# Kernel optimization log

Measured on AMD Instinct MI355X. Metric: run time of the kernel, lower is better.

The kernel has to match this reference:

```python
import jax, jax.numpy as jnp
import numpy as np

SEQ_LEN = 4096
DIM_HALF = 2048  # x last dim = 2 * DIM_HALF
DIM_OUT = 1024
LN_EPS = 1e-5


def setup_inputs() -> dict:
    key = jax.random.key(0)
    k1, k2, k3 = jax.random.split(key, 3)
    x = jax.random.normal(k1, (SEQ_LEN, 2 * DIM_HALF), dtype=jnp.float32)
    ln_scale = jnp.ones((DIM_HALF,), dtype=jnp.float32)
    # original init is uniform(-eps/n, eps/n); scale randn similarly small
    spatial_weights = jax.random.normal(k2, (SEQ_LEN, SEQ_LEN), dtype=jnp.float32) * (0.001 / SEQ_LEN)
    spatial_biases = jnp.ones((SEQ_LEN, 1), dtype=jnp.float32)
    proj_w = jax.random.normal(k3, (DIM_HALF, DIM_OUT), dtype=jnp.float32) * (1.0 / np.sqrt(DIM_HALF))
    proj_b = jnp.zeros((DIM_OUT,), dtype=jnp.float32)
    return {"x": x, "ln_scale": ln_scale, "spatial_weights": spatial_weights,
            "spatial_biases": spatial_biases, "proj_w": proj_w, "proj_b": proj_b}


def reference(x, ln_scale, spatial_weights, spatial_biases, proj_w, proj_b):
    # split into value half and gate half
    xh, gate = jnp.split(x, 2, axis=-1)  # each (n, d)
    # LayerNorm (scale only, no offset), haiku default eps=1e-5
    mean = jnp.mean(gate, axis=-1, keepdims=True)
    var = jnp.var(gate, axis=-1, keepdims=True)
    gate = (gate - mean) * jax.lax.rsqrt(var + LN_EPS) * ln_scale
    # causal (lower-triangular) masked spatial mixing: out[m,d] = sum_n w[m,n] * gate[n,d]
    n = spatial_weights.shape[0]
    w = jnp.tril(spatial_weights)
    gate = jnp.einsum('nd,mn->md', gate, w) + spatial_biases  # (n, d)
    # gating multiply + output projection
    out = (xh * gate) @ proj_w + proj_b  # (n, dim_out)
    return out
```

## Files before the change

### kernel.cpp

```cpp
#include <hip/hip_runtime.h>
#include <cstdint>
#include <cstddef>

#define SEQ 4096
#define DH 2048
#define DOUT 1024

typedef float f32x4 __attribute__((ext_vector_type(4)));
typedef __bf16 bf16x8 __attribute__((ext_vector_type(8)));
typedef long longx2 __attribute__((ext_vector_type(2)));


__device__ __forceinline__ unsigned short f2bf(float f) {
  unsigned int u = __float_as_uint(f);
  unsigned int r = (u + 0x7FFFu + ((u >> 16) & 1u)) >> 16;
  return (unsigned short)r;
}

__device__ __forceinline__ unsigned char f2f8(float f) {
  unsigned int u = __float_as_uint(f);
  unsigned int sign = (u >> 24) & 0x80u;
  float a = __uint_as_float(u & 0x7FFFFFFFu);
  if (a >= 448.f) return (unsigned char)(sign | 0x7Eu);
  if (a < 0.015625f) {
    int q = (int)rintf(a * 512.0f);
    if (q == 8) return (unsigned char)(sign | 0x08u);
    return (unsigned char)(sign | (unsigned)q);
  }
  int e = (int)((u >> 23) & 0xFF) - 127;
  unsigned int m = u & 0x7FFFFFu;
  unsigned int m3 = (m + 0x7FFFFu + ((m >> 20) & 1u)) >> 20;
  if (m3 == 8u) { m3 = 0u; e++; if (e > 8) return (unsigned char)(sign | 0x7Eu); }
  return (unsigned char)(sign | ((unsigned)(e + 7) << 3) | m3);
}

__device__ __forceinline__ void g2l16(const void* g, void* l) {
  __builtin_amdgcn_global_load_lds((__attribute__((address_space(1))) void*)g,
                                   (__attribute__((address_space(3))) void*)l, 16, 0, 0);
}

#define W_SCALE 1048576.0f
#define W_SCALE_INV (1.0f / 1048576.0f)


__global__ __launch_bounds__(256) void prep_all(const float* __restrict__ x,
                                                float* __restrict__ mv,
                                                float* __restrict__ rv,
                                                const float* __restrict__ w,
                                                unsigned char* __restrict__ wf8,
                                                const float* __restrict__ pw,
                                                unsigned short* __restrict__ pT) {
  int b = blockIdx.x;
  if (b < 4096) {
    int row = b;
    const float4* g4 = (const float4*)(x + (size_t)row * (2 * DH) + DH);
    float4 a = g4[threadIdx.x];
    float4 bb = g4[threadIdx.x + 256];
    float s  = a.x + a.y + a.z + a.w + bb.x + bb.y + bb.z + bb.w;
    float s2 = a.x * a.x + a.y * a.y + a.z * a.z + a.w * a.w +
               bb.x * bb.x + bb.y * bb.y + bb.z * bb.z + bb.w * bb.w;
#pragma unroll
    for (int o = 32; o > 0; o >>= 1) {
      s  += __shfl_down(s, o);
      s2 += __shfl_down(s2, o);
    }
    __shared__ float red[8];
    int wave = threadIdx.x >> 6;
    if ((threadIdx.x & 63) == 0) { red[wave] = s; red[wave + 4] = s2; }
    __syncthreads();
    if (threadIdx.x == 0) {
      float S  = red[0] + red[1] + red[2] + red[3];
      float S2 = red[4] + red[5] + red[6] + red[7];
      float mean = S * (1.0f / DH);
      float var  = S2 * (1.0f / DH) - mean * mean;
      mv[row] = mean;
      rv[row] = rsqrtf(var + 1e-5f);
    }
  } else if (b < 8192) {
    size_t e = (((size_t)(b - 4096)) * 256 + threadIdx.x) * 16;
    int m = (int)(e >> 12);
    int k = (int)(e & 4095);
    uint4 o;
    if (k > m) {
      o.x = o.y = o.z = o.w = 0u;
    } else {
      const float4* s4 = (const float4*)(w + e);
      float4 v0 = s4[0], v1 = s4[1], v2 = s4[2], v3 = s4[3];
      float vv[16] = {v0.x, v0.y, v0.z, v0.w, v1.x, v1.y, v1.z, v1.w,
                      v2.x, v2.y, v2.z, v2.w, v3.x, v3.y, v3.z, v3.w};
      unsigned char t[16];
#pragma unroll
      for (int j = 0; j < 16; j++)
        t[j] = (k + j <= m) ? f2f8(vv[j] * W_SCALE) : (unsigned char)0;
      o.x = (unsigned)t[0] | ((unsigned)t[1] << 8) | ((unsigned)t[2] << 16) | ((unsigned)t[3] << 24);
      o.y = (unsigned)t[4] | ((unsigned)t[5] << 8) | ((unsigned)t[6] << 16) | ((unsigned)t[7] << 24);
      o.z = (unsigned)t[8] | ((unsigned)t[9] << 8) | ((unsigned)t[10] << 16) | ((unsigned)t[11] << 24);
      o.w = (unsigned)t[12] | ((unsigned)t[13] << 8) | ((unsigned)t[14] << 16) | ((unsigned)t[15] << 24);
    }
    *(uint4*)(wf8 + e) = o;
  } else {
    __shared__ float tile[64][65];
    int b2 = b - 8192;
    int j0 = (b2 & 15) * 64;
    int d0 = (b2 >> 4) * 64;
#pragma unroll
    for (int i = 0; i < 16; i++) {
      int idx = threadIdx.x + i * 256;
      int r = idx >> 6, c = idx & 63;
      tile[r][c] = pw[(size_t)(d0 + r) * DOUT + j0 + c];
    }
    __syncthreads();
#pragma unroll
    for (int i = 0; i < 16; i++) {
      int idx = threadIdx.x + i * 256;
      int jr = idx >> 6, dc = idx & 63;
      pT[(size_t)(j0 + jr) * DH + d0 + dc] = f2bf(tile[dc][jr]);
    }
  }
}


__global__ __launch_bounds__(256) void norm_tr8(const float* __restrict__ x,
                                                const float* __restrict__ mv,
                                                const float* __restrict__ rv,
                                                const float* __restrict__ lns,
                                                unsigned char* __restrict__ gf8T) {
  __shared__ float tile[64][65];
  int d0 = blockIdx.x * 64;
  int n0 = blockIdx.y * 64;
#pragma unroll
  for (int i = 0; i < 16; i++) {
    int idx = threadIdx.x + i * 256;
    int r = idx >> 6, c = idx & 63;
    float v = x[(size_t)(n0 + r) * (2 * DH) + DH + d0 + c];
    tile[r][c] = (v - mv[n0 + r]) * rv[n0 + r];
  }
  __syncthreads();
#pragma unroll
  for (int i = 0; i < 4; i++) {
    int idx = threadIdx.x + i * 256;
    int dr = idx >> 4;
    int nq = idx & 15;
    float sc = lns[d0 + dr];
    unsigned int pk = 0;
#pragma unroll
    for (int j = 0; j < 4; j++)
      pk |= (unsigned int)f2f8(tile[nq * 4 + j][dr] * sc) << (8 * j);
    *(unsigned int*)&gf8T[(size_t)(d0 + dr) * SEQ + n0 + nq * 4] = pk;
  }
}


__global__ __launch_bounds__(256) void gemm_f8(const unsigned char* __restrict__ A,
                                               const unsigned char* __restrict__ BT,
                                               const float* __restrict__ xfull,
                                               const float* __restrict__ rbias,
                                               unsigned short* __restrict__ Pout) {
  constexpr int BK = 128;
  constexpr int ASZ = 64 * BK;
  __shared__ unsigned char sA[2 * ASZ];
  __shared__ unsigned char sB[2 * ASZ];

  const int tid = threadIdx.x;
  const int lane = tid & 63, wave = tid >> 6;
  const int quad = lane >> 4, l16 = lane & 15;
  const int wm = wave >> 1, wn = wave & 1;
  const int K = SEQ;

  const int lin = blockIdx.x;
  const int sw = ((lin & 7) << 7) | (lin >> 3);
  const int bn0 = (sw >> 5) * 64;
  const int by0 = sw & 31;

  for (int pass = 0; pass < 2; pass++) {
    const int by = pass == 0 ? by0 : 63 - by0;
    const int bm0 = by * 64;
    const int nt = (by + 2) >> 1;

    const unsigned char* aP[2];
    const unsigned char* bP[2];
#pragma unroll
    for (int r = 0; r < 2; r++) {
      int idx = r * 256 + tid;
      int row = idx >> 3;
      int col = ((idx & 7) ^ (row & 7)) * 16;
      aP[r] = A + (size_t)(bm0 + row) * K + col;
      bP[r] = BT + (size_t)(bn0 + row) * K + col;
    }

    f32x4 acc[2][2] = {};

    auto stage = [&](int buf) {
#pragma unroll
      for (int r = 0; r < 2; r++) {
        g2l16(aP[r], &sA[buf * ASZ + (r * 256 + tid) * 16]);
        aP[r] += BK;
      }
#pragma unroll
      for (int r = 0; r < 2; r++) {
        g2l16(bP[r], &sB[buf * ASZ + (r * 256 + tid) * 16]);
        bP[r] += BK;
      }
    };

    auto compute = [&](int buf) {
      const unsigned char* bA = &sA[buf * ASZ];
      const unsigned char* bB = &sB[buf * ASZ];
      long a8[4][2], b8[4][2];
#pragma unroll
      for (int i = 0; i < 2; i++) {
        int R = wm * 32 + i * 16 + l16;
        const unsigned char* rowp = &bA[R * BK];
        int s = R & 7;
        longx2 X = *(const longx2*)&rowp[(quad ^ s) * 16];
        longx2 Y = *(const longx2*)&rowp[((quad + 4) ^ s) * 16];
        a8[0][i] = X[0]; a8[1][i] = X[1]; a8[2][i] = Y[0]; a8[3][i] = Y[1];
      }
#pragma unroll
      for (int j = 0; j < 2; j++) {
        int R = wn * 32 + j * 16 + l16;
        const unsigned char* rowp = &bB[R * BK];
        int s = R & 7;
        longx2 X = *(const longx2*)&rowp[(quad ^ s) * 16];
        longx2 Y = *(const longx2*)&rowp[((quad + 4) ^ s) * 16];
        b8[0][j] = X[0]; b8[1][j] = X[1]; b8[2][j] = Y[0]; b8[3][j] = Y[1];
      }
#pragma unroll
      for (int h = 0; h < 4; h++)
#pragma unroll
        for (int i = 0; i < 2; i++)
#pragma unroll
          for (int j = 0; j < 2; j++)
            acc[i][j] = __builtin_amdgcn_mfma_f32_16x16x32_fp8_fp8(a8[h][i], b8[h][j], acc[i][j], 0, 0, 0);
    };

    stage(0);
    int cur = 0;
    for (int t = 0; t < nt; t++) {
      if (t + 1 < nt) {
        stage(cur ^ 1);
        asm volatile("s_waitcnt vmcnt(4)" ::: "memory");
      } else {
        asm volatile("s_waitcnt vmcnt(0)" ::: "memory");
      }
      __builtin_amdgcn_s_barrier();
      compute(cur);
      __builtin_amdgcn_s_barrier();
      cur ^= 1;
    }

#pragma unroll
    for (int i = 0; i < 2; i++) {
#pragma unroll
      for (int j = 0; j < 2; j++) {
        int col = bn0 + wn * 32 + j * 16 + l16;
#pragma unroll
        for (int r = 0; r < 4; r++) {
          int row = bm0 + wm * 32 + i * 16 + quad * 4 + r;
          float g = acc[i][j][r] * W_SCALE_INV + rbias[row];
          float pv = xfull[(size_t)row * (2 * DH) + col] * g;
          Pout[(size_t)row * DH + col] = f2bf(pv);
        }
      }
    }
  }
}


__global__ __launch_bounds__(256) void gemm_bf(const unsigned short* __restrict__ A,
                                               const unsigned short* __restrict__ BT,
                                               const float* __restrict__ cbias,
                                               float* __restrict__ out,
                                               int N, int K) {
  constexpr int BK = 64;
  constexpr int ASZ = 64 * BK;
  __shared__ unsigned short sA[2 * ASZ];
  __shared__ unsigned short sB[2 * ASZ];

  const int tid = threadIdx.x;
  const int lane = tid & 63, wave = tid >> 6;
  const int quad = lane >> 4, l16 = lane & 15;
  const int wm = wave >> 1, wn = wave & 1;

  const int lin = blockIdx.x;
  const int sw = ((lin & 7) << 7) | (lin >> 3);
  const int bn0 = (sw & 15) * 64;
  const int bm0 = (sw >> 4) * 64;
  const int nt = K / BK;

  const unsigned short* aP[2];
  const unsigned short* bP[2];
#pragma unroll
  for (int r = 0; r < 2; r++) {
    int idx = r * 256 + tid;
    int row = idx >> 3;
    int col = ((idx & 7) ^ (row & 7)) * 8;
    aP[r] = A + (size_t)(bm0 + row) * K + col;
    bP[r] = BT + (size_t)(bn0 + row) * K + col;
  }

  f32x4 acc[2][2] = {};

  auto stage = [&](int buf) {
#pragma unroll
    for (int r = 0; r < 2; r++) {
      g2l16(aP[r], &sA[buf * ASZ + (r * 256 + tid) * 8]);
      aP[r] += BK;
    }
#pragma unroll
    for (int r = 0; r < 2; r++) {
      g2l16(bP[r], &sB[buf * ASZ + (r * 256 + tid) * 8]);
      bP[r] += BK;
    }
  };

  auto compute = [&](int buf) {
    const unsigned short* bA = &sA[buf * ASZ];
    const unsigned short* bB = &sB[buf * ASZ];
    bf16x8 af[2][2], bfr[2][2];
#pragma unroll
    for (int h = 0; h < 2; h++) {
#pragma unroll
      for (int i = 0; i < 2; i++) {
        int R = wm * 32 + i * 16 + l16;
        af[h][i] = *(const bf16x8*)&bA[R * BK + (((h * 4 + quad) ^ (R & 7)) * 8)];
      }
#pragma unroll
      for (int j = 0; j < 2; j++) {
        int R = wn * 32 + j * 16 + l16;
        bfr[h][j] = *(const bf16x8*)&bB[R * BK + (((h * 4 + quad) ^ (R & 7)) * 8)];
      }
    }
#pragma unroll
    for (int h = 0; h < 2; h++)
#pragma unroll
      for (int i = 0; i < 2; i++)
#pragma unroll
        for (int j = 0; j < 2; j++)
          acc[i][j] = __builtin_amdgcn_mfma_f32_16x16x32_bf16(af[h][i], bfr[h][j], acc[i][j], 0, 0, 0);
  };

  stage(0);
  int cur = 0;
  for (int t = 0; t < nt; t++) {
    if (t + 1 < nt) {
      stage(cur ^ 1);
      asm volatile("s_waitcnt vmcnt(4)" ::: "memory");
    } else {
      asm volatile("s_waitcnt vmcnt(0)" ::: "memory");
    }
    __builtin_amdgcn_s_barrier();
    compute(cur);
    __builtin_amdgcn_s_barrier();
    cur ^= 1;
  }

#pragma unroll
  for (int i = 0; i < 2; i++) {
#pragma unroll
    for (int j = 0; j < 2; j++) {
      int col = bn0 + wn * 32 + j * 16 + l16;
#pragma unroll
      for (int r = 0; r < 4; r++) {
        int row = bm0 + wm * 32 + i * 16 + quad * 4 + r;
        out[(size_t)row * N + col] = acc[i][j][r] + cbias[col];
      }
    }
  }
}


extern "C" void kernel_launch(void* const* d_in, const int* in_sizes, int n_in,
                              void* d_out, int out_size, void* d_ws, size_t ws_size,
                              hipStream_t stream) {
  (void)in_sizes; (void)n_in; (void)out_size; (void)ws_size;
  const float* x   = (const float*)d_in[0];
  const float* lns = (const float*)d_in[1];
  const float* w   = (const float*)d_in[2];
  const float* sb  = (const float*)d_in[3];
  const float* pw  = (const float*)d_in[4];
  const float* pb  = (const float*)d_in[5];
  float* out = (float*)d_out;

  char* p = (char*)d_ws;
  unsigned char*  wf8   = (unsigned char*)p;  p += (size_t)SEQ * SEQ;
  unsigned char*  gf8T  = (unsigned char*)p;  p += (size_t)DH * SEQ;
  unsigned short* projT = (unsigned short*)p; p += (size_t)DOUT * DH * 2;
  unsigned short* Pbuf  = (unsigned short*)p; p += (size_t)SEQ * DH * 2;
  float* mv = (float*)p; p += (size_t)SEQ * 4;
  float* rv = (float*)p; p += (size_t)SEQ * 4;

  prep_all<<<4096 + 4096 + 512, 256, 0, stream>>>(x, mv, rv, w, wf8, pw, projT);
  norm_tr8<<<dim3(DH / 64, SEQ / 64), 256, 0, stream>>>(x, mv, rv, lns, gf8T);

  gemm_f8<<<1024, 256, 0, stream>>>(wf8, gf8T, x, sb, Pbuf);

  gemm_bf<<<1024, 256, 0, stream>>>(Pbuf, projT, pb, out, DOUT, DH);
}
```

Before: 232.6 us.

## Use hardware fp8 pack conversion and merge normalize-transpose into weight prep kernel

```diff
diff --git a/kernel.cpp b/kernel.cpp
--- a/kernel.cpp
+++ b/kernel.cpp
@@ -17,7 +17,7 @@
   return (unsigned short)r;
 }
 
-__device__ __forceinline__ unsigned char f2f8(float f) {
+__device__ __forceinline__ unsigned char f2f8_sw(float f) {
   unsigned int u = __float_as_uint(f);
   unsigned int sign = (u >> 24) & 0x80u;
   float a = __uint_as_float(u & 0x7FFFFFFFu);
@@ -34,6 +34,17 @@
   return (unsigned char)(sign | ((unsigned)(e + 7) << 3) | m3);
 }
 
+__device__ __forceinline__ unsigned int pk4_f8(float a, float b, float c, float d) {
+#if __has_builtin(__builtin_amdgcn_cvt_pk_fp8_f32)
+  int r = __builtin_amdgcn_cvt_pk_fp8_f32(a, b, 0, false);
+  r = __builtin_amdgcn_cvt_pk_fp8_f32(c, d, r, true);
+  return (unsigned int)r;
+#else
+  return (unsigned)f2f8_sw(a) | ((unsigned)f2f8_sw(b) << 8) |
+         ((unsigned)f2f8_sw(c) << 16) | ((unsigned)f2f8_sw(d) << 24);
+#endif
+}
+
 __device__ __forceinline__ void g2l16(const void* g, void* l) {
   __builtin_amdgcn_global_load_lds((__attribute__((address_space(1))) void*)g,
                                    (__attribute__((address_space(3))) void*)l, 16, 0, 0);
@@ -43,41 +54,70 @@
 #define W_SCALE_INV (1.0f / 1048576.0f)
 
 
-__global__ __launch_bounds__(256) void prep_all(const float* __restrict__ x,
+__global__ __launch_bounds__(256) void ln_stats(const float* __restrict__ x,
                                                 float* __restrict__ mv,
-                                                float* __restrict__ rv,
-                                                const float* __restrict__ w,
-                                                unsigned char* __restrict__ wf8,
-                                                const float* __restrict__ pw,
-                                                unsigned short* __restrict__ pT) {
+                                                float* __restrict__ rv) {
+  int row = blockIdx.x;
+  const float4* g4 = (const float4*)(x + (size_t)row * (2 * DH) + DH);
+  float4 a = g4[threadIdx.x];
+  float4 b = g4[threadIdx.x + 256];
+  float s  = a.x + a.y + a.z + a.w + b.x + b.y + b.z + b.w;
+  float s2 = a.x * a.x + a.y * a.y + a.z * a.z + a.w * a.w +
+             b.x * b.x + b.y * b.y + b.z * b.z + b.w * b.w;
+#pragma unroll
+  for (int o = 32; o > 0; o >>= 1) {
+    s  += __shfl_down(s, o);
+    s2 += __shfl_down(s2, o);
+  }
+  __shared__ float red[8];
+  int wave = threadIdx.x >> 6;
+  if ((threadIdx.x & 63) == 0) { red[wave] = s; red[wave + 4] = s2; }
+  __syncthreads();
+  if (threadIdx.x == 0) {
+    float S  = red[0] + red[1] + red[2] + red[3];
+    float S2 = red[4] + red[5] + red[6] + red[7];
+    float mean = S * (1.0f / DH);
+    float var  = S2 * (1.0f / DH) - mean * mean;
+    mv[row] = mean;
+    rv[row] = rsqrtf(var + 1e-5f);
+  }
+}
+
+
+__global__ __launch_bounds__(256) void prep2(const float* __restrict__ x,
+                                             const float* __restrict__ mv,
+                                             const float* __restrict__ rv,
+                                             const float* __restrict__ lns,
+                                             unsigned char* __restrict__ gf8T,
+                                             const float* __restrict__ w,
+                                             unsigned char* __restrict__ wf8,
+                                             const float* __restrict__ pw,
+                                             unsigned short* __restrict__ pT) {
   int b = blockIdx.x;
-  if (b < 4096) {
-    int row = b;
-    const float4* g4 = (const float4*)(x + (size_t)row * (2 * DH) + DH);
-    float4 a = g4[threadIdx.x];
-    float4 bb = g4[threadIdx.x + 256];
-    float s  = a.x + a.y + a.z + a.w + bb.x + bb.y + bb.z + bb.w;
-    float s2 = a.x * a.x + a.y * a.y + a.z * a.z + a.w * a.w +
-               bb.x * bb.x + bb.y * bb.y + bb.z * bb.z + bb.w * bb.w;
-#pragma unroll
-    for (int o = 32; o > 0; o >>= 1) {
-      s  += __shfl_down(s, o);
-      s2 += __shfl_down(s2, o);
-    }
-    __shared__ float red[8];
-    int wave = threadIdx.x >> 6;
-    if ((threadIdx.x & 63) == 0) { red[wave] = s; red[wave + 4] = s2; }
+  if (b < 2048) {
+    __shared__ float tile[64][65];
+    int d0 = (b & 31) * 64;
+    int n0 = (b >> 5) * 64;
+#pragma unroll
+    for (int i = 0; i < 16; i++) {
+      int idx = threadIdx.x + i * 256;
+      int r = idx >> 6, c = idx & 63;
+      float v = x[(size_t)(n0 + r) * (2 * DH) + DH + d0 + c];
+      tile[r][c] = (v - mv[n0 + r]) * rv[n0 + r];
+    }
     __syncthreads();
-    if (threadIdx.x == 0) {
-      float S  = red[0] + red[1] + red[2] + red[3];
-      float S2 = red[4] + red[5] + red[6] + red[7];
-      float mean = S * (1.0f / DH);
-      float var  = S2 * (1.0f / DH) - mean * mean;
-      mv[row] = mean;
-      rv[row] = rsqrtf(var + 1e-5f);
-    }
-  } else if (b < 8192) {
-    size_t e = (((size_t)(b - 4096)) * 256 + threadIdx.x) * 16;
+#pragma unroll
+    for (int i = 0; i < 4; i++) {
+      int idx = threadIdx.x + i * 256;
+      int dr = idx >> 4;
+      int nq = idx & 15;
+      float sc = lns[d0 + dr];
+      unsigned int pk = pk4_f8(tile[nq * 4 + 0][dr] * sc, tile[nq * 4 + 1][dr] * sc,
+                               tile[nq * 4 + 2][dr] * sc, tile[nq * 4 + 3][dr] * sc);
+      *(unsigned int*)&gf8T[(size_t)(d0 + dr) * SEQ + n0 + nq * 4] = pk;
+    }
+  } else if (b < 6144) {
+    size_t e = (((size_t)(b - 2048)) * 256 + threadIdx.x) * 16;
     int m = (int)(e >> 12);
     int k = (int)(e & 4095);
     uint4 o;
@@ -88,19 +128,19 @@
       float4 v0 = s4[0], v1 = s4[1], v2 = s4[2], v3 = s4[3];
       float vv[16] = {v0.x, v0.y, v0.z, v0.w, v1.x, v1.y, v1.z, v1.w,
                       v2.x, v2.y, v2.z, v2.w, v3.x, v3.y, v3.z, v3.w};
-      unsigned char t[16];
-#pragma unroll
-      for (int j = 0; j < 16; j++)
-        t[j] = (k + j <= m) ? f2f8(vv[j] * W_SCALE) : (unsigned char)0;
-      o.x = (unsigned)t[0] | ((unsigned)t[1] << 8) | ((unsigned)t[2] << 16) | ((unsigned)t[3] << 24);
-      o.y = (unsigned)t[4] | ((unsigned)t[5] << 8) | ((unsigned)t[6] << 16) | ((unsigned)t[7] << 24);
-      o.z = (unsigned)t[8] | ((unsigned)t[9] << 8) | ((unsigned)t[10] << 16) | ((unsigned)t[11] << 24);
-      o.w = (unsigned)t[12] | ((unsigned)t[13] << 8) | ((unsigned)t[14] << 16) | ((unsigned)t[15] << 24);
+      if (k + 15 > m) {
+#pragma unroll
+        for (int j = 0; j < 16; j++) vv[j] = (k + j <= m) ? vv[j] : 0.0f;
+      }
+      o.x = pk4_f8(vv[0] * W_SCALE, vv[1] * W_SCALE, vv[2] * W_SCALE, vv[3] * W_SCALE);
+      o.y = pk4_f8(vv[4] * W_SCALE, vv[5] * W_SCALE, vv[6] * W_SCALE, vv[7] * W_SCALE);
+      o.z = pk4_f8(vv[8] * W_SCALE, vv[9] * W_SCALE, vv[10] * W_SCALE, vv[11] * W_SCALE);
+      o.w = pk4_f8(vv[12] * W_SCALE, vv[13] * W_SCALE, vv[14] * W_SCALE, vv[15] * W_SCALE);
     }
     *(uint4*)(wf8 + e) = o;
   } else {
     __shared__ float tile[64][65];
-    int b2 = b - 8192;
+    int b2 = b - 6144;
     int j0 = (b2 & 15) * 64;
     int d0 = (b2 >> 4) * 64;
 #pragma unroll
@@ -116,37 +156,6 @@
       int jr = idx >> 6, dc = idx & 63;
       pT[(size_t)(j0 + jr) * DH + d0 + dc] = f2bf(tile[dc][jr]);
     }
-  }
-}
-
-
-__global__ __launch_bounds__(256) void norm_tr8(const float* __restrict__ x,
-                                                const float* __restrict__ mv,
-                                                const float* __restrict__ rv,
-                                                const float* __restrict__ lns,
-                                                unsigned char* __restrict__ gf8T) {
-  __shared__ float tile[64][65];
-  int d0 = blockIdx.x * 64;
-  int n0 = blockIdx.y * 64;
-#pragma unroll
-  for (int i = 0; i < 16; i++) {
-    int idx = threadIdx.x + i * 256;
-    int r = idx >> 6, c = idx & 63;
-    float v = x[(size_t)(n0 + r) * (2 * DH) + DH + d0 + c];
-    tile[r][c] = (v - mv[n0 + r]) * rv[n0 + r];
-  }
-  __syncthreads();
-#pragma unroll
-  for (int i = 0; i < 4; i++) {
-    int idx = threadIdx.x + i * 256;
-    int dr = idx >> 4;
-    int nq = idx & 15;
-    float sc = lns[d0 + dr];
-    unsigned int pk = 0;
-#pragma unroll
-    for (int j = 0; j < 4; j++)
-      pk |= (unsigned int)f2f8(tile[nq * 4 + j][dr] * sc) << (8 * j);
-    *(unsigned int*)&gf8T[(size_t)(d0 + dr) * SEQ + n0 + nq * 4] = pk;
   }
 }
 
@@ -390,8 +399,8 @@
   float* mv = (float*)p; p += (size_t)SEQ * 4;
   float* rv = (float*)p; p += (size_t)SEQ * 4;
 
-  prep_all<<<4096 + 4096 + 512, 256, 0, stream>>>(x, mv, rv, w, wf8, pw, projT);
-  norm_tr8<<<dim3(DH / 64, SEQ / 64), 256, 0, stream>>>(x, mv, rv, lns, gf8T);
+  ln_stats<<<SEQ, 256, 0, stream>>>(x, mv, rv);
+  prep2<<<2048 + 4096 + 512, 256, 0, stream>>>(x, mv, rv, lns, gf8T, w, wf8, pw, projT);
 
   gemm_f8<<<1024, 256, 0, stream>>>(wf8, gf8T, x, sb, Pbuf);
 
```

Measured after the change: 224.1 us. -3.6%, faster.
